# Kernel tuning notes

Measured on AMD Instinct MI355X. Metric: run time of the kernel, lower is better.

The kernel has to match this reference:

```python
import jax, jax.numpy as jnp
import numpy as np

G, DIN, DOUT, R = 8, 1024, 1024, 16
N = 8192
SCALE = 32.0 / 16.0  # alpha / r


def grouped_linear(x, W, mask):
    """Grouped linear: out[n] = x[n] @ W[g[n]].
    x: [N, din], W: [G, din, dout], mask: [N, G] one-hot (float).
    Computed as all-group matmul + select; the fused grouped-GEMM is the
    kernel opportunity this reference baselines."""
    y_all = jnp.einsum('ni,gio->gno', x, W)      # [G, N, dout]
    return jnp.einsum('gno,ng->no', y_all, mask)  # [N, dout]


def setup_inputs() -> dict:
    key = jax.random.key(0)
    k1, k2, k3, k4, k5 = jax.random.split(key, 5)
    x = jax.random.normal(k1, (N, DIN), dtype=jnp.float32)
    x_groups = jnp.sort(jax.random.randint(k2, (N,), 0, G, dtype=jnp.int64))
    W_base = jax.random.normal(k3, (G, DIN, DOUT), dtype=jnp.float32) * 0.02
    W_A = jax.random.normal(k4, (G, DIN, R), dtype=jnp.float32) * 0.02
    # original inits lora_B to zero; use small random values so the LoRA path
    # contributes nonzero signal for correctness testing
    W_B = jax.random.normal(k5, (G, R, DOUT), dtype=jnp.float32) * 0.02
    return {"x": x, "x_groups": x_groups, "W_base": W_base, "W_A": W_A, "W_B": W_B}


def reference(x, x_groups, W_base, W_A, W_B):
    mask = (x_groups[:, None] == jnp.arange(G)).astype(x.dtype)  # [N, G] one-hot
    base = grouped_linear(x, W_base, mask)            # base GroupedLinear
    a = grouped_linear(x, W_A, mask)                  # lora_A (dropout p=0 -> identity)
    adapt = grouped_linear(a, W_B, mask)              # lora_B
    return base + SCALE * adapt
```

## Files before the change

### kernel.cpp

```cpp
#include <hip/hip_runtime.h>
#include <stdint.h>

#define N_TOK 8192
#define DIN   1024
#define DOUT  1024
#define NG    8
#define LSCALE 2.0f

typedef __attribute__((ext_vector_type(4))) float  float4v;
typedef __attribute__((ext_vector_type(8))) short  short8;
typedef short8  frag_ab;
typedef float4v frag_cd;

__device__ __forceinline__ short f2bf(float f) {
    union { float f; uint32_t u; } v; v.f = f;
    uint32_t r = v.u + 0x7fffu + ((v.u >> 16) & 1u);
    return (short)(r >> 16);
}

__device__ __forceinline__ void load_lds16(const void* g, void* lds) {
    __builtin_amdgcn_global_load_lds(
        (const __attribute__((address_space(1))) uint32_t*)g,
        (__attribute__((address_space(3))) uint32_t*)lds,
        16, 0, 0);
}

#define PREP_GRID 6177

__global__ __launch_bounds__(256) void prep_kernel(
        const float* __restrict__ x, const float* __restrict__ Wb,
        const float* __restrict__ WA, const float* __restrict__ WB,
        const int* __restrict__ groups,
        short* __restrict__ xb, short* __restrict__ Wt,
        int* __restrict__ starts) {
    __shared__ float tile[64][65];
    __shared__ float At[64][17];
    __shared__ float Bt[16][64];
    const int blk = blockIdx.x, t = threadIdx.x;

    if (blk < 4096) {
        size_t idx = (size_t)(blk * 256 + t) * 8;
        const float4v* p = (const float4v*)(x + idx);
        float4v a = p[0], b = p[1];
        short8 o;
        o[0]=f2bf(a[0]); o[1]=f2bf(a[1]); o[2]=f2bf(a[2]); o[3]=f2bf(a[3]);
        o[4]=f2bf(b[0]); o[5]=f2bf(b[1]); o[6]=f2bf(b[2]); o[7]=f2bf(b[3]);
        *(short8*)(xb + idx) = o;
    } else if (blk < 6144) {
        int b = blk - 4096;
        int g = b >> 8, rem = b & 255;
        int n0 = (rem & 15) * 64, k0 = (rem >> 4) * 64;
        const float* Wg = Wb + (size_t)g * DIN * DOUT;
#pragma unroll
        for (int i = 0; i < 4; ++i) {
            int idx = i * 256 + t;
            int r = idx >> 4, c = (idx & 15) * 4;
            float4v v = *(const float4v*)(Wg + (size_t)(k0 + r) * DOUT + n0 + c);
            tile[r][c+0]=v[0]; tile[r][c+1]=v[1]; tile[r][c+2]=v[2]; tile[r][c+3]=v[3];
        }
        {
            int kk = t >> 2, c = (t & 3) * 4;
            float4v v = *(const float4v*)(WA + ((size_t)g * DIN + k0 + kk) * 16 + c);
            At[kk][c+0]=v[0]; At[kk][c+1]=v[1]; At[kk][c+2]=v[2]; At[kk][c+3]=v[3];
        }
        {
            int r = t >> 4, c = (t & 15) * 4;
            float4v v = *(const float4v*)(WB + ((size_t)g * 16 + r) * DOUT + n0 + c);
            Bt[r][c+0]=v[0]; Bt[r][c+1]=v[1]; Bt[r][c+2]=v[2]; Bt[r][c+3]=v[3];
        }
        __syncthreads();
        short* Wtg = Wt + (size_t)g * DOUT * DIN;
#pragma unroll
        for (int i = 0; i < 2; ++i) {
            int idx = i * 256 + t;
            int n = idx >> 3, c8 = (idx & 7) * 8;
            float corr[8] = {0.f,0.f,0.f,0.f,0.f,0.f,0.f,0.f};
#pragma unroll
            for (int r = 0; r < 16; ++r) {
                float bv = Bt[r][n];
#pragma unroll
                for (int j = 0; j < 8; ++j) corr[j] += At[c8 + j][r] * bv;
            }
            short8 o;
#pragma unroll
            for (int j = 0; j < 8; ++j)
                o[j] = f2bf(tile[c8 + j][n] + LSCALE * corr[j]);
            *(short8*)(Wtg + (size_t)(n0 + n) * DIN + k0 + c8) = o;
        }
    } else {
        int i = (blk - 6144) * 256 + t;
        if (i > N_TOK) return;
        int cur  = (i < N_TOK) ? groups[i] : NG;
        int prev = (i == 0) ? -1 : groups[i - 1];
        for (int g = prev + 1; g <= cur; ++g) starts[g] = i;
    }
}

#define BM 128
#define BN 128
#define BK 128
#define NKT (DIN / BK)

__global__ __launch_bounds__(256, 2)
void gemm_grouped(const short* __restrict__ xb,
                  const short* __restrict__ Wt,
                  const int*   __restrict__ starts,
                  float* __restrict__ out) {
    __shared__ short As[BM * BK];
    __shared__ short Bs[BN * BK];

    const int t    = threadIdx.x;
    const int lane = t & 63;
    const int wid  = t >> 6;
    const int L        = blockIdx.x;
    const int row_tile = (L & 7) * 8 + (L >> 6);
    const int col_tile = (L >> 3) & 7;
    const int col0 = col_tile * BN;
    const int row0 = row_tile * BM;
    const int wr   = (wid >> 1) * 64;
    const int wc   = (wid & 1) * 64;
    const int m16  = lane & 15;
    const int q    = lane >> 4;
    const int phase = ((L >> 3) & 1) * 4;

    int gbeg = 0;
    while (starts[gbeg + 1] <= row0) ++gbeg;

    for (int g = gbeg; g < NG && starts[g] < row0 + BM; ++g) {
        const int rlo = starts[g]     > row0      ? starts[g]     : row0;
        const int rhi = starts[g + 1] < row0 + BM ? starts[g + 1] : row0 + BM;
        if (rlo >= rhi) continue;

        const short* wg = Wt + (size_t)g * DOUT * DIN;

        frag_cd acc[4][4];
#pragma unroll
        for (int i = 0; i < 4; ++i)
#pragma unroll
            for (int j = 0; j < 4; ++j) { frag_cd z = {0.f,0.f,0.f,0.f}; acc[i][j] = z; }

        for (int kt_ii = 0; kt_ii < NKT; ++kt_ii) {
            const int kt = ((kt_ii + phase) & (NKT - 1)) * BK;

#pragma unroll
            for (int i = 0; i < 8; ++i) {
                int Lc = i * 256 + t;
                int r  = Lc >> 4;
                int c8 = (Lc & 15) ^ (r & 7);
                load_lds16(xb + (size_t)(row0 + r) * DIN + kt + c8 * 8,
                           &As[(i * 256 + wid * 64) * 8]);
            }
#pragma unroll
            for (int i = 0; i < 8; ++i) {
                int Lc = i * 256 + t;
                int r  = Lc >> 4;
                int c8 = (Lc & 15) ^ (r & 7);
                load_lds16(wg + (size_t)(col0 + r) * DIN + kt + c8 * 8,
                           &Bs[(i * 256 + wid * 64) * 8]);
            }
            __syncthreads();

#pragma unroll
            for (int kk = 0; kk < BK; kk += 32) {
                frag_ab af[4], bf[4];
                const int ch = (kk >> 3) + q;
#pragma unroll
                for (int mi = 0; mi < 4; ++mi) {
                    int rr = wr + mi * 16 + m16;
                    af[mi] = *(const frag_ab*)&As[rr * BK + ((ch ^ (rr & 7)) << 3)];
                }
#pragma unroll
                for (int ni = 0; ni < 4; ++ni) {
                    int cc = wc + ni * 16 + m16;
                    bf[ni] = *(const frag_ab*)&Bs[cc * BK + ((ch ^ (cc & 7)) << 3)];
                }
#pragma unroll
                for (int mi = 0; mi < 4; ++mi)
#pragma unroll
                    for (int ni = 0; ni < 4; ++ni)
                        acc[mi][ni] = __builtin_amdgcn_mfma_f32_16x16x32_bf16(
                            af[mi], bf[ni], acc[mi][ni], 0, 0, 0);
            }
            __syncthreads();
        }

#pragma unroll
        for (int mi = 0; mi < 4; ++mi)
#pragma unroll
            for (int r = 0; r < 4; ++r) {
                int grow = row0 + wr + mi * 16 + q * 4 + r;
                if (grow >= rlo && grow < rhi) {
                    float* orow = out + (size_t)grow * DOUT + col0 + wc + m16;
#pragma unroll
                    for (int ni = 0; ni < 4; ++ni) orow[ni * 16] = acc[mi][ni][r];
                }
            }
    }
}

extern "C" void kernel_launch(void* const* d_in, const int* in_sizes, int n_in,
                              void* d_out, int out_size, void* d_ws, size_t ws_size,
                              hipStream_t stream) {
    const float* x      = (const float*)d_in[0];
    const int*   groups = (const int*)d_in[1];
    const float* Wb     = (const float*)d_in[2];
    const float* WA     = (const float*)d_in[3];
    const float* WB     = (const float*)d_in[4];
    float* out = (float*)d_out;

    char* ws = (char*)d_ws;
    int*   starts = (int*)ws;
    short* xb     = (short*)(ws + 1024);
    short* Wt     = (short*)(ws + 1024 + (size_t)16 * 1024 * 1024);

    hipLaunchKernelGGL(prep_kernel, dim3(PREP_GRID), dim3(256), 0, stream,
                       x, Wb, WA, WB, groups, xb, Wt, starts);
    hipLaunchKernelGGL(gemm_grouped, dim3(512), dim3(256), 0, stream,
                       xb, Wt, starts, out);
}
```

Baseline: 153.7 us.

## Assign GEMM tiles per group and double-buffer LDS staging with BK=64

Builds the tile list from group boundaries so each block computes one group for up to 128 rows. This avoids running the full K loop twice for tiles that straddle a group boundary. It also switches to a two-stage LDS buffer with a smaller K tile, so the next tile's global-to-LDS loads overlap the current tile's MFMAs. The grid grows to cover the worst-case number of group tiles, and unused blocks exit early. Group-aligned tiles may read rows beyond the group end, which are masked on store.

```diff
diff --git a/kernel.cpp b/kernel.cpp
--- a/kernel.cpp
+++ b/kernel.cpp
@@ -98,104 +98,123 @@
 
 #define BM 128
 #define BN 128
-#define BK 128
+#define BK 64
 #define NKT (DIN / BK)
+#define MAXRT (N_TOK / BM + NG - 1)
+#define GRID  (MAXRT * (DOUT / BN))
 
 __global__ __launch_bounds__(256, 2)
 void gemm_grouped(const short* __restrict__ xb,
                   const short* __restrict__ Wt,
                   const int*   __restrict__ starts,
                   float* __restrict__ out) {
-    __shared__ short As[BM * BK];
-    __shared__ short Bs[BN * BK];
+    __shared__ short As[2][BM * BK];
+    __shared__ short Bs[2][BN * BK];
 
     const int t    = threadIdx.x;
     const int lane = t & 63;
     const int wid  = t >> 6;
-    const int L        = blockIdx.x;
-    const int row_tile = (L & 7) * 8 + (L >> 6);
-    const int col_tile = (L >> 3) & 7;
-    const int col0 = col_tile * BN;
-    const int row0 = row_tile * BM;
-    const int wr   = (wid >> 1) * 64;
-    const int wc   = (wid & 1) * 64;
-    const int m16  = lane & 15;
-    const int q    = lane >> 4;
-    const int phase = ((L >> 3) & 1) * 4;
-
-    int gbeg = 0;
-    while (starts[gbeg + 1] <= row0) ++gbeg;
-
-    for (int g = gbeg; g < NG && starts[g] < row0 + BM; ++g) {
-        const int rlo = starts[g]     > row0      ? starts[g]     : row0;
-        const int rhi = starts[g + 1] < row0 + BM ? starts[g + 1] : row0 + BM;
-        if (rlo >= rhi) continue;
-
-        const short* wg = Wt + (size_t)g * DOUT * DIN;
-
-        frag_cd acc[4][4];
-#pragma unroll
-        for (int i = 0; i < 4; ++i)
-#pragma unroll
-            for (int j = 0; j < 4; ++j) { frag_cd z = {0.f,0.f,0.f,0.f}; acc[i][j] = z; }
-
-        for (int kt_ii = 0; kt_ii < NKT; ++kt_ii) {
-            const int kt = ((kt_ii + phase) & (NKT - 1)) * BK;
-
-#pragma unroll
-            for (int i = 0; i < 8; ++i) {
-                int Lc = i * 256 + t;
-                int r  = Lc >> 4;
-                int c8 = (Lc & 15) ^ (r & 7);
-                load_lds16(xb + (size_t)(row0 + r) * DIN + kt + c8 * 8,
-                           &As[(i * 256 + wid * 64) * 8]);
-            }
-#pragma unroll
-            for (int i = 0; i < 8; ++i) {
-                int Lc = i * 256 + t;
-                int r  = Lc >> 4;
-                int c8 = (Lc & 15) ^ (r & 7);
-                load_lds16(wg + (size_t)(col0 + r) * DIN + kt + c8 * 8,
-                           &Bs[(i * 256 + wid * 64) * 8]);
-            }
-            __syncthreads();
-
-#pragma unroll
-            for (int kk = 0; kk < BK; kk += 32) {
-                frag_ab af[4], bf[4];
-                const int ch = (kk >> 3) + q;
-#pragma unroll
-                for (int mi = 0; mi < 4; ++mi) {
-                    int rr = wr + mi * 16 + m16;
-                    af[mi] = *(const frag_ab*)&As[rr * BK + ((ch ^ (rr & 7)) << 3)];
-                }
-#pragma unroll
-                for (int ni = 0; ni < 4; ++ni) {
-                    int cc = wc + ni * 16 + m16;
-                    bf[ni] = *(const frag_ab*)&Bs[cc * BK + ((ch ^ (cc & 7)) << 3)];
-                }
-#pragma unroll
-                for (int mi = 0; mi < 4; ++mi)
-#pragma unroll
-                    for (int ni = 0; ni < 4; ++ni)
-                        acc[mi][ni] = __builtin_amdgcn_mfma_f32_16x16x32_bf16(
-                            af[mi], bf[ni], acc[mi][ni], 0, 0, 0);
-            }
-            __syncthreads();
-        }
-
-#pragma unroll
-        for (int mi = 0; mi < 4; ++mi)
-#pragma unroll
-            for (int r = 0; r < 4; ++r) {
-                int grow = row0 + wr + mi * 16 + q * 4 + r;
-                if (grow >= rlo && grow < rhi) {
-                    float* orow = out + (size_t)grow * DOUT + col0 + wc + m16;
-#pragma unroll
-                    for (int ni = 0; ni < 4; ++ni) orow[ni * 16] = acc[mi][ni][r];
-                }
-            }
+    const int L  = blockIdx.x;
+    const int wg = (L & 7) * MAXRT + (L >> 3);
+    const int rt = wg >> 3;
+    const int ct = wg & 7;
+    const int col0 = ct * BN;
+
+    int g = -1, row0 = 0, rhi = 0;
+    {
+        int accum = 0;
+#pragma unroll
+        for (int gg = 0; gg < NG; ++gg) {
+            int s0 = starts[gg], s1 = starts[gg + 1];
+            int nt = (s1 - s0 + BM - 1) >> 7;
+            if (g < 0 && rt < accum + nt) {
+                g = gg;
+                row0 = s0 + (rt - accum) * BM;
+                rhi = (s1 < row0 + BM) ? s1 : row0 + BM;
+            }
+            accum += nt;
+        }
     }
+    if (g < 0) return;
+
+    const short* wgp = Wt + (size_t)g * DOUT * DIN;
+    const int wr  = (wid >> 1) * 64;
+    const int wc  = (wid & 1) * 64;
+    const int m16 = lane & 15;
+    const int q   = lane >> 4;
+    const int phase = ((L >> 3) & 1) * 8;
+
+    frag_cd acc[4][4];
+#pragma unroll
+    for (int i = 0; i < 4; ++i)
+#pragma unroll
+        for (int j = 0; j < 4; ++j) { frag_cd z = {0.f,0.f,0.f,0.f}; acc[i][j] = z; }
+
+    auto STAGE = [&](int buf, int kt) {
+#pragma unroll
+        for (int i = 0; i < 4; ++i) {
+            int Lc = i * 256 + t;
+            int r  = Lc >> 3;
+            int c8 = (Lc & 7) ^ (r & 7);
+            load_lds16(xb + (size_t)(row0 + r) * DIN + kt + c8 * 8,
+                       &As[buf][(i * 256 + wid * 64) * 8]);
+        }
+#pragma unroll
+        for (int i = 0; i < 4; ++i) {
+            int Lc = i * 256 + t;
+            int r  = Lc >> 3;
+            int c8 = (Lc & 7) ^ (r & 7);
+            load_lds16(wgp + (size_t)(col0 + r) * DIN + kt + c8 * 8,
+                       &Bs[buf][(i * 256 + wid * 64) * 8]);
+        }
+    };
+
+    STAGE(0, ((0 + phase) & (NKT - 1)) * BK);
+    __syncthreads();
+
+    int cur = 0;
+#pragma unroll 2
+    for (int kt_ii = 0; kt_ii < NKT; ++kt_ii) {
+        if (kt_ii + 1 < NKT)
+            STAGE(cur ^ 1, ((kt_ii + 1 + phase) & (NKT - 1)) * BK);
+
+#pragma unroll
+        for (int kk = 0; kk < BK; kk += 32) {
+            frag_ab af[4], bf[4];
+            const int ch = (kk >> 3) + q;
+#pragma unroll
+            for (int mi = 0; mi < 4; ++mi) {
+                int rr = wr + mi * 16 + m16;
+                af[mi] = *(const frag_ab*)&As[cur][rr * BK + ((ch ^ (rr & 7)) << 3)];
+            }
+#pragma unroll
+            for (int ni = 0; ni < 4; ++ni) {
+                int cc = wc + ni * 16 + m16;
+                bf[ni] = *(const frag_ab*)&Bs[cur][cc * BK + ((ch ^ (cc & 7)) << 3)];
+            }
+#pragma unroll
+            for (int mi = 0; mi < 4; ++mi)
+#pragma unroll
+                for (int ni = 0; ni < 4; ++ni)
+                    acc[mi][ni] = __builtin_amdgcn_mfma_f32_16x16x32_bf16(
+                        af[mi], bf[ni], acc[mi][ni], 0, 0, 0);
+        }
+
+        __syncthreads();
+        cur ^= 1;
+    }
+
+#pragma unroll
+    for (int mi = 0; mi < 4; ++mi)
+#pragma unroll
+        for (int r = 0; r < 4; ++r) {
+            int grow = row0 + wr + mi * 16 + q * 4 + r;
+            if (grow < rhi) {
+                float* orow = out + (size_t)grow * DOUT + col0 + wc + m16;
+#pragma unroll
+                for (int ni = 0; ni < 4; ++ni) orow[ni * 16] = acc[mi][ni][r];
+            }
+        }
 }
 
 extern "C" void kernel_launch(void* const* d_in, const int* in_sizes, int n_in,
@@ -215,6 +234,6 @@
 
     hipLaunchKernelGGL(prep_kernel, dim3(PREP_GRID), dim3(256), 0, stream,
                        x, Wb, WA, WB, groups, xb, Wt, starts);
-    hipLaunchKernelGGL(gemm_grouped, dim3(512), dim3(256), 0, stream,
+    hipLaunchKernelGGL(gemm_grouped, dim3(GRID), dim3(256), 0, stream,
                        xb, Wt, starts, out);
 }
```

Measured after the change: 155.5 us. No clear change (+1.2%).
